# Kernel tuning notes

Measured on AMD Instinct MI355X. Metric: run time of the kernel, lower is better.

The kernel has to match this reference:

```python
import jax, jax.numpy as jnp
import numpy as np

B, S, R, L, Z = 2048, 277, 80, 12, 56


def setup_inputs() -> dict:
    key = jax.random.key(0)
    k0, k1, k2, k3, k4, k5 = jax.random.split(key, 6)
    true_idx = jax.random.randint(k0, (B, S), 0, R)
    x = jax.nn.one_hot(true_idx, R, dtype=jnp.float32)            # one-hot true rules
    recon_x = jax.nn.softmax(jax.random.normal(k1, (B, S, R)), axis=-1)  # post-softmax probs
    mu = jax.random.normal(k2, (B, Z), dtype=jnp.float32)
    log_var = jax.random.normal(k3, (B, Z), dtype=jnp.float32)
    ind_to_lhs_ind = jax.random.randint(k4, (R,), 0, L)
    masks = (jax.random.uniform(k5, (L, R)) > 0.5).astype(jnp.float32)
    # a valid grammar always allows the true rule under its own LHS mask
    masks = masks.at[ind_to_lhs_ind, jnp.arange(R)].set(1.0)
    return {"x": x, "recon_x": recon_x, "mu": mu, "log_var": log_var,
            "masks": masks, "ind_to_lhs_ind": ind_to_lhs_ind}


def reference(x, recon_x, mu, log_var, masks, ind_to_lhs_ind):
    batch_size, seq_len, n_rules = x.shape
    z_size = mu.shape[1]
    # apply_masks: fused gather + mask + renormalize (replaces B*S python loop)
    true_rule = jnp.argmax(x, axis=-1)                 # [B,S]
    mask = masks[ind_to_lhs_ind[true_rule]]            # [B,S,R]
    x_resc = recon_x * mask
    out = x_resc / jnp.sum(x_resc, axis=-1, keepdims=True)
    # BCELoss(size_average=False): torch clamps log terms at -100
    log_p = jnp.clip(jnp.log(out), -100.0, None)
    log_1mp = jnp.clip(jnp.log1p(-out), -100.0, None)
    bce = -jnp.sum(x * log_p + (1.0 - x) * log_1mp) / (seq_len * batch_size)
    # sample_z == False branch: moment-matching error
    avg_mu = jnp.sum(mu, axis=0) / batch_size          # [Z]
    var = jnp.matmul(mu.T, mu) / batch_size            # [Z,Z]
    var_err = var - jnp.eye(z_size, dtype=mu.dtype)
    mom_err = jnp.sum(avg_mu * avg_mu) / z_size + jnp.sum(jnp.abs(var_err)) / (z_size * z_size)
    return bce + mom_err
```

## Files before the change

kernel.cpp:

```cpp
#include <hip/hip_runtime.h>
#include <math.h>

#define Bn 2048
#define Sn 277
#define Rn 80
#define Ln 12
#define Zn 56
#define NROWS (Bn * Sn)
#define ROWS_PER_BLK 256
#define NBLK_BCE (NROWS / ROWS_PER_BLK)
#define NMOM 8
#define NBLK_TOT (NBLK_BCE + NMOM)
#define NWAVE_BCE (NBLK_BCE * 4)

#define WS_CM  0
#define WS_BCE 1280
#define WS_VAR 36736
#define WS_AVG 49280

__device__ __forceinline__ float qsum4(float v) {
    int t = __builtin_amdgcn_update_dpp(0, __float_as_int(v), 0xB1, 0xF, 0xF, true);
    v += __int_as_float(t);
    t = __builtin_amdgcn_update_dpp(0, __float_as_int(v), 0x4E, 0xF, 0xF, true);
    v += __int_as_float(t);
    return v;
}

__global__ __launch_bounds__(256) void setup_kernel(
    const float* __restrict__ masks, const int* __restrict__ lhs, char* __restrict__ ws)
{
    unsigned* cmask_sw = (unsigned*)(ws + WS_CM);
    for (int idx = threadIdx.x; idx < Rn * 4; idx += 256) {
        const int r = idx >> 2, c = idx & 3;
        const int l = lhs[r];
        unsigned bits = 0u;
        for (int k = 0; k < 5; ++k)
            for (int comp = 0; comp < 4; ++comp) {
                const int j = 16 * k + 4 * c + comp;
                if (masks[l * Rn + j] > 0.5f) bits |= (1u << (4 * k + comp));
            }
        cmask_sw[idx] = bits;
    }
}

__global__ __launch_bounds__(256, 2) void main_kernel(
    const float* __restrict__ x, const float* __restrict__ recon,
    const float* __restrict__ mu, char* __restrict__ ws)
{
    const int tid = threadIdx.x;

    if (blockIdx.x < NMOM) {
        float* var_g = (float*)(ws + WS_VAR);
        float* avg_g = (float*)(ws + WS_AVG);
        __shared__ float sm[32 * Zn];

        const int m = blockIdx.x;
        float acc[13];
        #pragma unroll
        for (int k = 0; k < 13; ++k) acc[k] = 0.0f;
        float asum = 0.0f;

        for (int ch = 0; ch < 8; ++ch) {
            __syncthreads();
            const float* src = mu + ((size_t)m * 256 + ch * 32) * Zn;
            #pragma unroll
            for (int i = 0; i < 7; ++i) sm[tid + 256 * i] = src[tid + 256 * i];
            __syncthreads();

            #pragma unroll
            for (int k = 0; k < 13; ++k) {
                const int p = tid + 256 * k;
                if (p < Zn * Zn) {
                    const int i = p / Zn, j = p - i * Zn;
                    float a = 0.0f;
                    #pragma unroll 8
                    for (int r = 0; r < 32; ++r) a = fmaf(sm[r * Zn + i], sm[r * Zn + j], a);
                    acc[k] += a;
                }
            }
            if (tid < Zn) {
                float s = 0.0f;
                #pragma unroll 8
                for (int r = 0; r < 32; ++r) s += sm[r * Zn + tid];
                asum += s;
            }
        }
        #pragma unroll
        for (int k = 0; k < 13; ++k) {
            const int p = tid + 256 * k;
            if (p < Zn * Zn) atomicAdd(&var_g[p], acc[k]);
        }
        if (tid < Zn) atomicAdd(&avg_g[tid], asum);
        return;
    }

    const int bid = blockIdx.x - NMOM;
    const unsigned* cmask_sw = (const unsigned*)(ws + WS_CM);
    float* bce_partial = (float*)(ws + WS_BCE);

    const int q = tid >> 2;
    const int c = tid & 3;
    const size_t row0 = (size_t)bid * ROWS_PER_BLK + 4 * (size_t)q;
    const float4* xp0 = (const float4*)(x + row0 * Rn);
    const float4* rp0 = (const float4*)(recon + row0 * Rn);

    float4 X[4][5], Rv[4][5];
    #pragma unroll
    for (int j = 0; j < 4; ++j)
        #pragma unroll
        for (int k = 0; k < 5; ++k)
            X[j][k] = xp0[20 * j + c + 4 * k];
    #pragma unroll
    for (int j = 0; j < 4; ++j)
        #pragma unroll
        for (int k = 0; k < 5; ++k)
            Rv[j][k] = rp0[20 * j + c + 4 * k];
    __builtin_amdgcn_sched_barrier(0);

    auto dotc = [](const float4 v, float base) {
        return fmaf(v.x, base, fmaf(v.y, base + 1.f, fmaf(v.z, base + 2.f, v.w * (base + 3.f))));
    };

    float ss = 0.0f;
    #pragma unroll
    for (int j = 0; j < 4; ++j) {
        float dl = dotc(X[j][0], 0.f) + dotc(X[j][1], 16.f) + dotc(X[j][2], 32.f)
                 + dotc(X[j][3], 48.f) + dotc(X[j][4], 64.f);
        float xs = 0.f;
        #pragma unroll
        for (int k = 0; k < 5; ++k)
            xs += ((X[j][k].x + X[j][k].y) + (X[j][k].z + X[j][k].w));
        dl = fmaf((float)(4 * c), xs, dl);
        const int amax = (int)(qsum4(dl) + 0.5f);

        const unsigned bits = cmask_sw[(amax << 2) | c];

        float4 M[5];
        #pragma unroll
        for (int k = 0; k < 5; ++k) {
            M[k].x = ((bits >> (4 * k + 0)) & 1u) ? Rv[j][k].x : 0.f;
            M[k].y = ((bits >> (4 * k + 1)) & 1u) ? Rv[j][k].y : 0.f;
            M[k].z = ((bits >> (4 * k + 2)) & 1u) ? Rv[j][k].z : 0.f;
            M[k].w = ((bits >> (4 * k + 3)) & 1u) ? Rv[j][k].w : 0.f;
        }
        float dd = 0.f;
        #pragma unroll
        for (int k = 0; k < 5; ++k)
            dd += ((M[k].x + M[k].y) + (M[k].z + M[k].w));
        const float invd = __builtin_amdgcn_rcpf(qsum4(dd));

        const int ka = amax >> 4;
        const int ca = (amax >> 2) & 3;
        const int comp = amax & 3;
        const bool owner = (c == ca);

        float p = 1.0f;
        float ta = 1.0f;
        #pragma unroll
        for (int k = 0; k < 5; ++k) {
            const float t0 = fminf(M[k].x * invd, 1.f);
            const float t1 = fminf(M[k].y * invd, 1.f);
            const float t2 = fminf(M[k].z * invd, 1.f);
            const float t3 = fminf(M[k].w * invd, 1.f);
            p *= ((1.f - t0) * (1.f - t1)) * ((1.f - t2) * (1.f - t3));
            if (owner && k == ka)
                ta = (comp == 0) ? t0 : (comp == 1) ? t1 : (comp == 2) ? t2 : t3;
        }
        if (p > 0.0f) {
            ss += __builtin_amdgcn_logf(p) * 0.69314718055994531f;
        } else {
            const float4* rpj = rp0 + 20 * j;
            #pragma unroll
            for (int k = 0; k < 5; ++k) {
                const float4 v = rpj[c + 4 * k];
                const float w0 = ((bits >> (4 * k + 0)) & 1u) ? v.x : 0.f;
                const float w1 = ((bits >> (4 * k + 1)) & 1u) ? v.y : 0.f;
                const float w2 = ((bits >> (4 * k + 2)) & 1u) ? v.z : 0.f;
                const float w3 = ((bits >> (4 * k + 3)) & 1u) ? v.w : 0.f;
                ss += fmaxf(__logf(1.f - fminf(w0 * invd, 1.f)), -100.f)
                    + fmaxf(__logf(1.f - fminf(w1 * invd, 1.f)), -100.f)
                    + fmaxf(__logf(1.f - fminf(w2 * invd, 1.f)), -100.f)
                    + fmaxf(__logf(1.f - fminf(w3 * invd, 1.f)), -100.f);
            }
        }
        if (owner)
            ss += fmaxf(__logf(ta), -100.f) - fmaxf(__logf(1.f - ta), -100.f);
    }

    ss = qsum4(ss);
    ss += __shfl_xor(ss, 4);
    ss += __shfl_xor(ss, 8);
    ss += __shfl_xor(ss, 16);
    ss += __shfl_xor(ss, 32);
    if ((tid & 63) == 0)
        bce_partial[bid * 4 + (tid >> 6)] = ss;
}

__global__ __launch_bounds__(256) void finalize_kernel(
    const char* __restrict__ ws, float* __restrict__ out)
{
    const float* bce_partial = (const float*)(ws + WS_BCE);
    const float* var_g = (const float*)(ws + WS_VAR);
    const float* avg_g = (const float*)(ws + WS_AVG);
    __shared__ double sb[4];
    __shared__ float sv[4], sa[4];
    const int tid = threadIdx.x;

    double bsum = 0.0;
    for (int i = tid; i < NWAVE_BCE; i += 256) bsum += (double)bce_partial[i];

    float vsum = 0.0f;
    for (int p = tid; p < Zn * Zn; p += 256) {
        const int i = p / Zn, j = p - i * Zn;
        const float e = var_g[p] * (1.0f / (float)Bn) - ((i == j) ? 1.0f : 0.0f);
        vsum += fabsf(e);
    }
    float asum = 0.0f;
    for (int z = tid; z < Zn; z += 256) { const float a = avg_g[z]; asum += a * a; }

    #pragma unroll
    for (int o = 32; o; o >>= 1) {
        bsum += __shfl_xor(bsum, o);
        vsum += __shfl_xor(vsum, o);
        asum += __shfl_xor(asum, o);
    }
    if ((tid & 63) == 0) { const int w = tid >> 6; sb[w] = bsum; sv[w] = vsum; sa[w] = asum; }
    __syncthreads();
    if (tid == 0) {
        const double tb = (sb[0] + sb[1]) + (sb[2] + sb[3]);
        const double tv = (double)((sv[0] + sv[1]) + (sv[2] + sv[3]));
        const double ta = (double)((sa[0] + sa[1]) + (sa[2] + sa[3]));
        const double bce = -tb / ((double)Sn * (double)Bn);
        const double mom = ta / ((double)Bn * (double)Bn * (double)Zn)
                         + tv / ((double)Zn * (double)Zn);
        out[0] = (float)(bce + mom);
    }
}

extern "C" void kernel_launch(void* const* d_in, const int* in_sizes, int n_in,
                              void* d_out, int out_size, void* d_ws, size_t ws_size,
                              hipStream_t stream)
{
    const float* x     = (const float*)d_in[0];
    const float* recon = (const float*)d_in[1];
    const float* mu    = (const float*)d_in[2];
    const float* masks = (const float*)d_in[4];
    const int*   lhs   = (const int*)d_in[5];
    float* out = (float*)d_out;
    char* ws = (char*)d_ws;

    hipMemsetAsync(ws + WS_VAR, 0, 12544 + 224, stream);
    setup_kernel<<<1, 256, 0, stream>>>(masks, lhs, ws);
    main_kernel<<<NBLK_TOT, 256, 0, stream>>>(x, recon, mu, ws);
    finalize_kernel<<<1, 256, 0, stream>>>(ws, out);
}
```

Baseline: 383.1 us.

## Stage BCE tiles through LDS with coalesced loads and split moment work wider

The BCE blocks now handle 64 rows each. They load x and recon with fully coalesced float4 reads, stage them in padded LDS, and then each 4-lane group reads its own row, instead of doing strided per-thread global loads of four rows. Blocks reduce to one partial per block through LDS. The moment path is split across 32 blocks that each load their whole mu slice once. This trades extra LDS traffic, barriers and more blocks for better global coalescing, higher occupancy (launch bound 3), and better parallelism in the mu^T mu computation.

```diff
diff --git a/kernel.cpp b/kernel.cpp
--- a/kernel.cpp
+++ b/kernel.cpp
@@ -7,11 +7,11 @@
 #define Ln 12
 #define Zn 56
 #define NROWS (Bn * Sn)
-#define ROWS_PER_BLK 256
+#define ROWS_PER_BLK 64
 #define NBLK_BCE (NROWS / ROWS_PER_BLK)
-#define NMOM 8
+#define NMOM 32
+#define MROWS (Bn / NMOM)
 #define NBLK_TOT (NBLK_BCE + NMOM)
-#define NWAVE_BCE (NBLK_BCE * 4)
 
 #define WS_CM  0
 #define WS_BCE 1280
@@ -43,54 +43,45 @@
     }
 }
 
-__global__ __launch_bounds__(256, 2) void main_kernel(
+__global__ __launch_bounds__(256, 3) void main_kernel(
     const float* __restrict__ x, const float* __restrict__ recon,
     const float* __restrict__ mu, char* __restrict__ ws)
 {
+    __shared__ float4 ldsb[2688];
     const int tid = threadIdx.x;
 
     if (blockIdx.x < NMOM) {
         float* var_g = (float*)(ws + WS_VAR);
         float* avg_g = (float*)(ws + WS_AVG);
-        __shared__ float sm[32 * Zn];
-
+        float* sm = (float*)ldsb;
         const int m = blockIdx.x;
+        const float* src = mu + (size_t)m * MROWS * Zn;
+        for (int i = tid; i < MROWS * Zn; i += 256) sm[i] = src[i];
+        __syncthreads();
+
         float acc[13];
         #pragma unroll
-        for (int k = 0; k < 13; ++k) acc[k] = 0.0f;
-        float asum = 0.0f;
-
-        for (int ch = 0; ch < 8; ++ch) {
-            __syncthreads();
-            const float* src = mu + ((size_t)m * 256 + ch * 32) * Zn;
-            #pragma unroll
-            for (int i = 0; i < 7; ++i) sm[tid + 256 * i] = src[tid + 256 * i];
-            __syncthreads();
-
-            #pragma unroll
-            for (int k = 0; k < 13; ++k) {
-                const int p = tid + 256 * k;
-                if (p < Zn * Zn) {
-                    const int i = p / Zn, j = p - i * Zn;
-                    float a = 0.0f;
-                    #pragma unroll 8
-                    for (int r = 0; r < 32; ++r) a = fmaf(sm[r * Zn + i], sm[r * Zn + j], a);
-                    acc[k] += a;
-                }
+        for (int k = 0; k < 13; ++k) {
+            const int p = tid + 256 * k;
+            float a = 0.0f;
+            if (p < Zn * Zn) {
+                const int i = p / Zn, j = p - i * Zn;
+                #pragma unroll 8
+                for (int r = 0; r < MROWS; ++r) a = fmaf(sm[r * Zn + i], sm[r * Zn + j], a);
             }
-            if (tid < Zn) {
-                float s = 0.0f;
-                #pragma unroll 8
-                for (int r = 0; r < 32; ++r) s += sm[r * Zn + tid];
-                asum += s;
-            }
+            acc[k] = a;
         }
         #pragma unroll
         for (int k = 0; k < 13; ++k) {
             const int p = tid + 256 * k;
             if (p < Zn * Zn) atomicAdd(&var_g[p], acc[k]);
         }
-        if (tid < Zn) atomicAdd(&avg_g[tid], asum);
+        if (tid < Zn) {
+            float s = 0.0f;
+            #pragma unroll 8
+            for (int r = 0; r < MROWS; ++r) s += sm[r * Zn + tid];
+            atomicAdd(&avg_g[tid], s);
+        }
         return;
     }
 
@@ -98,38 +89,46 @@
     const unsigned* cmask_sw = (const unsigned*)(ws + WS_CM);
     float* bce_partial = (float*)(ws + WS_BCE);
 
-    const int q = tid >> 2;
-    const int c = tid & 3;
-    const size_t row0 = (size_t)bid * ROWS_PER_BLK + 4 * (size_t)q;
-    const float4* xp0 = (const float4*)(x + row0 * Rn);
-    const float4* rp0 = (const float4*)(recon + row0 * Rn);
-
-    float4 X[4][5], Rv[4][5];
-    #pragma unroll
-    for (int j = 0; j < 4; ++j)
+    const size_t base = (size_t)bid * (ROWS_PER_BLK * (Rn / 4));
+    const float4* xg = (const float4*)x + base;
+    const float4* rg = (const float4*)recon + base;
+
+    float4 tv[10];
+    #pragma unroll
+    for (int i = 0; i < 5; ++i) tv[i]     = xg[256 * i + tid];
+    #pragma unroll
+    for (int i = 0; i < 5; ++i) tv[5 + i] = rg[256 * i + tid];
+    #pragma unroll
+    for (int i = 0; i < 5; ++i) {
+        const int f = 256 * i + tid;
+        const int row = f / 20, col = f - 20 * row;
+        ldsb[row * 21 + col]        = tv[i];
+        ldsb[1344 + row * 21 + col] = tv[5 + i];
+    }
+    __syncthreads();
+
+    const int qq = tid >> 2;
+    const int c  = tid & 3;
+    const int sb = qq * 21 + c;
+
+    float4 X[5], Rv[5];
+    #pragma unroll
+    for (int k = 0; k < 5; ++k) X[k]  = ldsb[sb + 4 * k];
+    #pragma unroll
+    for (int k = 0; k < 5; ++k) Rv[k] = ldsb[1344 + sb + 4 * k];
+
+    auto dotc = [](const float4 v, float base_) {
+        return fmaf(v.x, base_, fmaf(v.y, base_ + 1.f, fmaf(v.z, base_ + 2.f, v.w * (base_ + 3.f))));
+    };
+
+    float ss = 0.0f;
+    {
+        float dl = dotc(X[0], 0.f) + dotc(X[1], 16.f) + dotc(X[2], 32.f)
+                 + dotc(X[3], 48.f) + dotc(X[4], 64.f);
+        float xs = 0.f;
         #pragma unroll
         for (int k = 0; k < 5; ++k)
-            X[j][k] = xp0[20 * j + c + 4 * k];
-    #pragma unroll
-    for (int j = 0; j < 4; ++j)
-        #pragma unroll
-        for (int k = 0; k < 5; ++k)
-            Rv[j][k] = rp0[20 * j + c + 4 * k];
-    __builtin_amdgcn_sched_barrier(0);
-
-    auto dotc = [](const float4 v, float base) {
-        return fmaf(v.x, base, fmaf(v.y, base + 1.f, fmaf(v.z, base + 2.f, v.w * (base + 3.f))));
-    };
-
-    float ss = 0.0f;
-    #pragma unroll
-    for (int j = 0; j < 4; ++j) {
-        float dl = dotc(X[j][0], 0.f) + dotc(X[j][1], 16.f) + dotc(X[j][2], 32.f)
-                 + dotc(X[j][3], 48.f) + dotc(X[j][4], 64.f);
-        float xs = 0.f;
-        #pragma unroll
-        for (int k = 0; k < 5; ++k)
-            xs += ((X[j][k].x + X[j][k].y) + (X[j][k].z + X[j][k].w));
+            xs += ((X[k].x + X[k].y) + (X[k].z + X[k].w));
         dl = fmaf((float)(4 * c), xs, dl);
         const int amax = (int)(qsum4(dl) + 0.5f);
 
@@ -138,10 +137,10 @@
         float4 M[5];
         #pragma unroll
         for (int k = 0; k < 5; ++k) {
-            M[k].x = ((bits >> (4 * k + 0)) & 1u) ? Rv[j][k].x : 0.f;
-            M[k].y = ((bits >> (4 * k + 1)) & 1u) ? Rv[j][k].y : 0.f;
-            M[k].z = ((bits >> (4 * k + 2)) & 1u) ? Rv[j][k].z : 0.f;
-            M[k].w = ((bits >> (4 * k + 3)) & 1u) ? Rv[j][k].w : 0.f;
+            M[k].x = ((bits >> (4 * k + 0)) & 1u) ? Rv[k].x : 0.f;
+            M[k].y = ((bits >> (4 * k + 1)) & 1u) ? Rv[k].y : 0.f;
+            M[k].z = ((bits >> (4 * k + 2)) & 1u) ? Rv[k].z : 0.f;
+            M[k].w = ((bits >> (4 * k + 3)) & 1u) ? Rv[k].w : 0.f;
         }
         float dd = 0.f;
         #pragma unroll
@@ -169,18 +168,12 @@
         if (p > 0.0f) {
             ss += __builtin_amdgcn_logf(p) * 0.69314718055994531f;
         } else {
-            const float4* rpj = rp0 + 20 * j;
             #pragma unroll
             for (int k = 0; k < 5; ++k) {
-                const float4 v = rpj[c + 4 * k];
-                const float w0 = ((bits >> (4 * k + 0)) & 1u) ? v.x : 0.f;
-                const float w1 = ((bits >> (4 * k + 1)) & 1u) ? v.y : 0.f;
-                const float w2 = ((bits >> (4 * k + 2)) & 1u) ? v.z : 0.f;
-                const float w3 = ((bits >> (4 * k + 3)) & 1u) ? v.w : 0.f;
-                ss += fmaxf(__logf(1.f - fminf(w0 * invd, 1.f)), -100.f)
-                    + fmaxf(__logf(1.f - fminf(w1 * invd, 1.f)), -100.f)
-                    + fmaxf(__logf(1.f - fminf(w2 * invd, 1.f)), -100.f)
-                    + fmaxf(__logf(1.f - fminf(w3 * invd, 1.f)), -100.f);
+                ss += fmaxf(__logf(1.f - fminf(M[k].x * invd, 1.f)), -100.f)
+                    + fmaxf(__logf(1.f - fminf(M[k].y * invd, 1.f)), -100.f)
+                    + fmaxf(__logf(1.f - fminf(M[k].z * invd, 1.f)), -100.f)
+                    + fmaxf(__logf(1.f - fminf(M[k].w * invd, 1.f)), -100.f);
             }
         }
         if (owner)
@@ -192,8 +185,12 @@
     ss += __shfl_xor(ss, 8);
     ss += __shfl_xor(ss, 16);
     ss += __shfl_xor(ss, 32);
-    if ((tid & 63) == 0)
-        bce_partial[bid * 4 + (tid >> 6)] = ss;
+    __syncthreads();
+    float* smf = (float*)ldsb;
+    if ((tid & 63) == 0) smf[tid >> 6] = ss;
+    __syncthreads();
+    if (tid == 0)
+        bce_partial[bid] = (smf[0] + smf[1]) + (smf[2] + smf[3]);
 }
 
 __global__ __launch_bounds__(256) void finalize_kernel(
@@ -207,7 +204,7 @@
     const int tid = threadIdx.x;
 
     double bsum = 0.0;
-    for (int i = tid; i < NWAVE_BCE; i += 256) bsum += (double)bce_partial[i];
+    for (int i = tid; i < NBLK_BCE; i += 256) bsum += (double)bce_partial[i];
 
     float vsum = 0.0f;
     for (int p = tid; p < Zn * Zn; p += 256) {
```

After: 377.2 us. Within noise of the previous version (-1.5%).
